# Kernel optimization log

Measured on AMD Instinct MI355X. Metric: run time of the kernel, lower is better.

## Reference

```python
import jax, jax.numpy as jnp
import numpy as np

N = 100000
E = 1600000
IN_F = 64
HID = 128
GC_OUT = 128
FEATS_OUT = 128


def _init_params(key):
    ks = jax.random.split(key, 6)
    s = 0.02
    return dict(
        W1=jax.random.normal(ks[0], (IN_F, HID), jnp.float32) * s,
        b1=jnp.zeros((HID,), jnp.float32),
        W2=jax.random.normal(ks[1], (HID, HID), jnp.float32) * s,
        b2=jnp.zeros((HID,), jnp.float32),
        Wgc=jax.random.normal(ks[2], (HID + IN_F, GC_OUT), jnp.float32) * s,
        bgc=jnp.zeros((GC_OUT,), jnp.float32),
        Wc=jax.random.normal(ks[3], (HID + GC_OUT, FEATS_OUT), jnp.float32) * s,
        bc=jnp.zeros((FEATS_OUT,), jnp.float32),
    )


def setup_inputs() -> dict:
    key = jax.random.key(0)
    k_f, k_e, k_p = jax.random.split(key, 3)
    inp = dict(
        feats=jax.random.normal(k_f, (N, IN_F), jnp.float32),
        edges=jax.random.randint(k_e, (2, E), 0, N, jnp.int64 if jax.config.read('jax_enable_x64') else jnp.int32),
        batch=jnp.zeros((N,), jnp.int32),
    )
    inp.update(_init_params(k_p))
    return inp


def _gcn_conv(x, edges, Wgc, bgc):
    # PyG GCNConv: linear transform, add self-loops, symmetric deg norm, scatter-add.
    n = x.shape[0]
    x = x @ Wgc  # [N, GC_OUT]
    loop = jnp.arange(n, dtype=edges.dtype)
    src = jnp.concatenate([edges[0], loop])
    dst = jnp.concatenate([edges[1], loop])
    deg = jax.ops.segment_sum(jnp.ones_like(dst, dtype=x.dtype), dst, num_segments=n)
    dinv = jnp.where(deg > 0, jax.lax.rsqrt(deg), 0.0)
    norm = dinv[src] * dinv[dst]  # [E+N]
    msg = x[src] * norm[:, None]  # gather + scale (memory-bound)
    agg = jax.ops.segment_sum(msg, dst, num_segments=n)  # scatter-add
    return agg + bgc


def reference(feats, edges, batch, W1, b1, W2, b2, Wgc, bgc, Wc, bc):
    elu = jax.nn.elu
    nfeats = elu(elu(feats @ W1 + b1) @ W2 + b2)  # fcnn
    gc_in = jnp.concatenate([nfeats, feats], axis=1)  # inject_input_to_gc
    gc_feats = _gcn_conv(gc_in, edges, Wgc, bgc)
    out_feats = elu(jnp.concatenate([nfeats, gc_feats], axis=1) @ Wc + bc)
    return (out_feats, edges, batch)
```

## Files before the change

### kernel.cpp

```cpp
#include <hip/hip_runtime.h>
#include <hip/hip_bf16.h>
#include <hip/hip_fp8.h>

constexpr int NN = 100000;
constexpr int NE = 1600000;

constexpr int SH1  = 9;
constexpr int NB1  = (NN + 511) >> SH1;
constexpr int EB   = 8192;
constexpr int NBLK = (NE + EB - 1) / EB;
constexpr int NH   = NB1 * NBLK;

constexpr float FP8_SCL  = 128.f;
constexpr float FP8_ISCL = 1.f / 128.f;

typedef __bf16 bf16_t;
typedef bf16_t bf16x8 __attribute__((ext_vector_type(8)));
typedef bf16_t bf16x4 __attribute__((ext_vector_type(4)));
typedef float  f32x4  __attribute__((ext_vector_type(4)));
typedef float  f32x2  __attribute__((ext_vector_type(2)));

__device__ inline float elu_fast(float v) {
  return v > 0.f ? v : (__expf(v) - 1.f);
}

__device__ inline unsigned char f_to_fp8(float v) {
  __hip_fp8_e4m3 q(v);
  return q.__x;
}
template<int SEL>
__device__ inline float fp8_to_f(unsigned int word) {
#if __has_builtin(__builtin_amdgcn_cvt_f32_fp8)
  return __builtin_amdgcn_cvt_f32_fp8(word, SEL);
#else
  __hip_fp8_e4m3 t; t.__x = (word >> (8 * SEL)) & 0xff; return (float)t;
#endif
}
template<bool W>
__device__ inline f32x2 fp8pk2(unsigned int word) {
#if __has_builtin(__builtin_amdgcn_cvt_pk_f32_fp8)
  return __builtin_amdgcn_cvt_pk_f32_fp8((int)word, W);
#else
  f32x2 o; o.x = fp8_to_f<W ? 2 : 0>(word); o.y = fp8_to_f<W ? 3 : 1>(word); return o;
#endif
}
__device__ inline void fp8x8_add(float* acc, uint2 v) {
  f32x2 p0 = fp8pk2<false>(v.x);
  f32x2 p1 = fp8pk2<true >(v.x);
  f32x2 p2 = fp8pk2<false>(v.y);
  f32x2 p3 = fp8pk2<true >(v.y);
  acc[0] += p0.x; acc[1] += p0.y;
  acc[2] += p1.x; acc[3] += p1.y;
  acc[4] += p2.x; acc[5] += p2.y;
  acc[6] += p3.x; acc[7] += p3.y;
}
__device__ inline void fp8x8_fma(float* acc, uint2 v, float s) {
  f32x2 p0 = fp8pk2<false>(v.x);
  f32x2 p1 = fp8pk2<true >(v.x);
  f32x2 p2 = fp8pk2<false>(v.y);
  f32x2 p3 = fp8pk2<true >(v.y);
  acc[0] += p0.x * s; acc[1] += p0.y * s;
  acc[2] += p1.x * s; acc[3] += p1.y * s;
  acc[4] += p2.x * s; acc[5] += p2.y * s;
  acc[6] += p3.x * s; acc[7] += p3.y * s;
}

constexpr int SB = 256;

__global__ void scan_blk(const int* __restrict__ in, int* __restrict__ incl,
                         int* __restrict__ bsum, int n) {
  __shared__ int sm[SB];
  int i = blockIdx.x * SB + threadIdx.x;
  int v = (i < n) ? in[i] : 0;
  sm[threadIdx.x] = v;
  __syncthreads();
  for (int off = 1; off < SB; off <<= 1) {
    int t = (threadIdx.x >= off) ? sm[threadIdx.x - off] : 0;
    __syncthreads();
    sm[threadIdx.x] += t;
    __syncthreads();
  }
  if (i < n) incl[i] = sm[threadIdx.x];
  if (threadIdx.x == SB - 1) bsum[blockIdx.x] = sm[SB - 1];
}

__global__ void scan_top(int* __restrict__ bsum, int nb) {
  __shared__ int sm[512];
  int t = threadIdx.x;
  int v = (t < nb) ? bsum[t] : 0;
  sm[t] = v;
  __syncthreads();
  for (int off = 1; off < 512; off <<= 1) {
    int u = (t >= off) ? sm[t - off] : 0;
    __syncthreads();
    sm[t] += u;
    __syncthreads();
  }
  if (t < nb) bsum[t] = sm[t] - v;
}

__global__ void scan_add(const int* __restrict__ incl, const int* __restrict__ in,
                         const int* __restrict__ bsum, int* __restrict__ outoff, int n) {
  int i = blockIdx.x * SB + threadIdx.x;
  if (i < n) {
    int off = bsum[blockIdx.x];
    outoff[i] = off + incl[i] - in[i];
    if (i == n - 1) outoff[n] = off + incl[i];
  }
}


__global__ __launch_bounds__(256) void histA(const int* __restrict__ dst,
                                             int* __restrict__ H, int e) {
  __shared__ int h[NB1];
  for (int i = threadIdx.x; i < NB1; i += 256) h[i] = 0;
  __syncthreads();
  int base = blockIdx.x * EB;
  int end = min(base + EB, e);
  for (int i = base + threadIdx.x; i < end; i += 256)
    atomicAdd(&h[dst[i] >> SH1], 1);
  __syncthreads();
  for (int i = threadIdx.x; i < NB1; i += 256)
    H[i * NBLK + blockIdx.x] = h[i];
}

__global__ void boff_k(const int* __restrict__ Hoff, int* __restrict__ boff) {
  int i = blockIdx.x * blockDim.x + threadIdx.x;
  if (i < NB1) boff[i] = Hoff[i * NBLK];
  if (i == NB1) boff[NB1] = NE;
}

__global__ __launch_bounds__(256) void scatterA(
    const int* __restrict__ src, const int* __restrict__ dst,
    const int* __restrict__ Hoff, unsigned long long* __restrict__ ebuf, int e) {
  __shared__ int cur[NB1];
  for (int i = threadIdx.x; i < NB1; i += 256)
    cur[i] = Hoff[i * NBLK + blockIdx.x];
  __syncthreads();
  int base = blockIdx.x * EB;
  int end = min(base + EB, e);
  for (int i = base + threadIdx.x; i < end; i += 256) {
    int d = dst[i], s = src[i];
    int pos = atomicAdd(&cur[d >> SH1], 1);
    ebuf[pos] = ((unsigned long long)(unsigned)d << 32) | (unsigned)s;
  }
}


__global__ __launch_bounds__(512) void bfin(const unsigned long long* __restrict__ ebuf,
                                            const int* __restrict__ boff,
                                            int* __restrict__ row_off, float* __restrict__ dinv,
                                            int* __restrict__ csr, int n) {
  __shared__ int cnt[512];
  __shared__ int loc[512];
  const int tid = threadIdx.x;
  const int b = blockIdx.x;
  cnt[tid] = 0;
  __syncthreads();
  const int e0 = boff[b], e1 = boff[b + 1];
  for (int e = e0 + tid; e < e1; e += 512)
    atomicAdd(&cnt[(int)(ebuf[e] >> 32) & 511], 1);
  __syncthreads();
  loc[tid] = cnt[tid];
  __syncthreads();
  for (int off = 1; off < 512; off <<= 1) {
    int t = (tid >= off) ? loc[tid - off] : 0;
    __syncthreads();
    loc[tid] += t;
    __syncthreads();
  }
  const int excl = loc[tid] - cnt[tid];
  const int node = (b << SH1) + tid;
  if (node < n) {
    row_off[node] = boff[b] + excl;
    dinv[node] = rsqrtf((float)cnt[tid] + 1.0f);
  }
  if (b == NB1 - 1 && tid == 0) row_off[n] = NE;
  cnt[tid] = boff[b] + excl;
  __syncthreads();
  for (int e = e0 + tid; e < e1; e += 512) {
    unsigned long long v = ebuf[e];
    int dl = (int)(v >> 32) & 511;
    int s  = (int)(v & 0xffffffffu);
    int slot = atomicAdd(&cnt[dl], 1);
    csr[slot] = s;
  }
}


__global__ void i2f4_k(const int4* __restrict__ in, float4* __restrict__ out, int n4) {
  int i = blockIdx.x * blockDim.x + threadIdx.x;
  if (i < n4) {
    int4 v = in[i];
    out[i] = make_float4((float)v.x, (float)v.y, (float)v.z, (float)v.w);
  }
}

__global__ void wprep4(const float* __restrict__ W1, const float* __restrict__ W2,
                       const float* __restrict__ Wgc, const float* __restrict__ Wc,
                       bf16_t* __restrict__ Wf) {
  int idx = blockIdx.x * blockDim.x + threadIdx.x;
  const float* W; int base;
  if      (idx < 8192)  { W = W1;  base = 0; }
  else if (idx < 24576) { W = W2;  base = 8192; }
  else if (idx < 49152) { W = Wgc; base = 24576; }
  else                  { W = Wc;  base = 49152; }
  int il   = idx - base;
  int j    = il & 7;
  int lane = (il >> 3) & 63;
  int c    = (il >> 9) & 7;
  int kt   = il >> 12;
  int k    = kt * 32 + (lane >> 4) * 8 + j;
  int col  = c * 16 + (lane & 15);
  Wf[idx] = (bf16_t)W[(size_t)k * 128 + col];
}

__global__ __launch_bounds__(256) void mf_dense123(
    const float* __restrict__ A, const bf16_t* __restrict__ W1f, const float* __restrict__ b1,
    const bf16_t* __restrict__ W2f, const float* __restrict__ b2,
    const bf16_t* __restrict__ Wgf, const float* __restrict__ dinv_g,
    bf16_t* __restrict__ h2out, unsigned char* __restrict__ xqout, int n)
{
  __shared__ __align__(16) char h1s[64 * 256];
  const int tid  = threadIdx.x;
  const int wv   = tid >> 6;
  const int lane = tid & 63;
  const int r    = lane & 15;
  const int kb   = lane >> 4;
  const int row0 = blockIdx.x * 64 + wv * 16;

  const bf16x8* W1V = (const bf16x8*)W1f;
  const bf16x8* W2V = (const bf16x8*)W2f;
  const bf16x8* WgV = (const bf16x8*)Wgf;

  f32x4 acc[8];
  #pragma unroll
  for (int c = 0; c < 8; ++c) acc[c] = (f32x4){0.f, 0.f, 0.f, 0.f};

  #pragma unroll
  for (int kt = 0; kt < 2; ++kt) {
    const int kofs = kt * 32 + kb * 8;
    int row = row0 + r; if (row >= n) row = n - 1;
    const float* fp = A + (size_t)row * 64 + kofs;
    float4 u = *(const float4*)fp;
    float4 v = *(const float4*)(fp + 4);
    bf16x8 a = (bf16x8){(bf16_t)u.x, (bf16_t)u.y, (bf16_t)u.z, (bf16_t)u.w,
                        (bf16_t)v.x, (bf16_t)v.y, (bf16_t)v.z, (bf16_t)v.w};
    #pragma unroll
    for (int c = 0; c < 8; ++c) {
      bf16x8 b = W1V[(kt * 8 + c) * 64 + lane];
      acc[c] = __builtin_amdgcn_mfma_f32_16x16x32_bf16(a, b, acc[c], 0, 0, 0);
    }
  }

  #pragma unroll
  for (int c = 0; c < 8; ++c) {
    const int col = c * 16 + r;
    const float bv = b1[col];
    #pragma unroll
    for (int q = 0; q < 4; ++q) {
      int rloc = wv * 16 + kb * 4 + q;
      float v = elu_fast(acc[c][q] + bv);
      int off = (rloc * 256 + col * 2) ^ ((rloc & 7) << 4);
      *(bf16_t*)(h1s + off) = (bf16_t)v;
    }
  }

  #pragma unroll
  for (int c = 0; c < 8; ++c) acc[c] = (f32x4){0.f, 0.f, 0.f, 0.f};

  #pragma unroll
  for (int kt = 0; kt < 4; ++kt) {
    const int kbyte = (kt * 32 + kb * 8) * 2;
    int rloc = wv * 16 + r;
    int off = (rloc * 256 + kbyte) ^ ((rloc & 7) << 4);
    bf16x8 a = *(const bf16x8*)(h1s + off);
    #pragma unroll
    for (int c = 0; c < 8; ++c) {
      bf16x8 b = W2V[(kt * 8 + c) * 64 + lane];
      acc[c] = __builtin_amdgcn_mfma_f32_16x16x32_bf16(a, b, acc[c], 0, 0, 0);
    }
  }

  #pragma unroll
  for (int c = 0; c < 8; ++c) {
    const int col = c * 16 + r;
    const float bv = b2[col];
    #pragma unroll
    for (int q = 0; q < 4; ++q) {
      int row  = row0 + kb * 4 + q;
      int rloc = wv * 16 + kb * 4 + q;
      float v = elu_fast(acc[c][q] + bv);
      int off = (rloc * 256 + col * 2) ^ ((rloc & 7) << 4);
      *(bf16_t*)(h1s + off) = (bf16_t)v;
      if (row < n) h2out[(size_t)row * 128 + col] = (bf16_t)v;
    }
  }

  #pragma unroll
  for (int c = 0; c < 8; ++c) acc[c] = (f32x4){0.f, 0.f, 0.f, 0.f};

  #pragma unroll
  for (int kt = 0; kt < 6; ++kt) {
    const int kofs = kt * 32 + kb * 8;
    bf16x8 a;
    if (kofs < 128) {
      int rloc = wv * 16 + r;
      int off = (rloc * 256 + kofs * 2) ^ ((rloc & 7) << 4);
      a = *(const bf16x8*)(h1s + off);
    } else {
      int row = row0 + r; if (row >= n) row = n - 1;
      const float* fp = A + (size_t)row * 64 + (kofs - 128);
      float4 u = *(const float4*)fp;
      float4 v = *(const float4*)(fp + 4);
      a = (bf16x8){(bf16_t)u.x, (bf16_t)u.y, (bf16_t)u.z, (bf16_t)u.w,
                   (bf16_t)v.x, (bf16_t)v.y, (bf16_t)v.z, (bf16_t)v.w};
    }
    #pragma unroll
    for (int c = 0; c < 8; ++c) {
      bf16x8 b = WgV[(kt * 8 + c) * 64 + lane];
      acc[c] = __builtin_amdgcn_mfma_f32_16x16x32_bf16(a, b, acc[c], 0, 0, 0);
    }
  }

  float dv[4];
  #pragma unroll
  for (int q = 0; q < 4; ++q) {
    int row = row0 + kb * 4 + q;
    dv[q] = (row < n) ? dinv_g[row] * FP8_SCL : 0.f;
  }
  #pragma unroll
  for (int c = 0; c < 8; ++c) {
    const int col = c * 16 + r;
    #pragma unroll
    for (int q = 0; q < 4; ++q) {
      int row = row0 + kb * 4 + q;
      if (row < n)
        xqout[(size_t)row * 128 + col] = f_to_fp8(acc[c][q] * dv[q]);
    }
  }
}

template<int K1, int K2, bool DOELU, int OMODE>
__global__ __launch_bounds__(256) void mf_dense(
    const bf16_t* __restrict__ A1, const bf16_t* __restrict__ A2b,
    const bf16_t* __restrict__ Wf, const float* __restrict__ bias,
    bf16_t* __restrict__ outb, float* __restrict__ outf, int n)
{
  constexpr int K   = K1 + K2;
  constexpr int NKT = K / 32;

  const int tid  = threadIdx.x;
  const int wv   = tid >> 6;
  const int lane = tid & 63;
  const int r    = lane & 15;
  const int kb   = lane >> 4;
  const int row0 = blockIdx.x * 64 + wv * 16;

  f32x4 acc[8];
  #pragma unroll
  for (int c = 0; c < 8; ++c) acc[c] = (f32x4){0.f, 0.f, 0.f, 0.f};

  const bf16x8* WfV = (const bf16x8*)Wf;

  #pragma unroll
  for (int kt = 0; kt < NKT; ++kt) {
    const int kofs = kt * 32 + kb * 8;
    int row = row0 + r; if (row >= n) row = n - 1;
    bf16x8 a;
    if (kofs < K1) a = *(const bf16x8*)(A1 + (size_t)row * K1 + kofs);
    else           a = *(const bf16x8*)(A2b + (size_t)row * K2 + (kofs - K1));
    #pragma unroll
    for (int c = 0; c < 8; ++c) {
      bf16x8 b = WfV[(kt * 8 + c) * 64 + lane];
      acc[c] = __builtin_amdgcn_mfma_f32_16x16x32_bf16(a, b, acc[c], 0, 0, 0);
    }
  }

  #pragma unroll
  for (int c = 0; c < 8; ++c) {
    const int col = c * 16 + r;
    const float bv = bias ? bias[col] : 0.f;
    #pragma unroll
    for (int q = 0; q < 4; ++q) {
      int row = row0 + kb * 4 + q;
      if (row < n) {
        float v = acc[c][q] + bv;
        if (DOELU) v = elu_fast(v);
        if (OMODE == 0) outb[(size_t)row * 128 + col] = (bf16_t)v;
        else            outf[(size_t)row * 128 + col] = v;
      }
    }
  }
}

__global__ __launch_bounds__(256) void gcn_agg6(
    const int* __restrict__ row_off, const int* __restrict__ csr,
    const float* __restrict__ dinv, const unsigned char* __restrict__ xq,
    const float* __restrict__ bgc, bf16_t* __restrict__ agg, int n)
{
  int w = (int)((blockIdx.x * (unsigned)blockDim.x + threadIdx.x) >> 6);
  if (w >= n) return;
  const int lane = threadIdx.x & 63;
  const int g  = lane >> 4;
  const int li = lane & 15;

  float acc[8];
  #pragma unroll
  for (int j = 0; j < 8; ++j) acc[j] = 0.f;

  if (g == 0) {
    uint2 sv = ((const uint2*)(xq + (size_t)w * 128))[li];
    fp8x8_add(acc, sv);
  }

  const int e0 = row_off[w], e1 = row_off[w + 1];
  int e = e0;
  for (; e + 16 <= e1; e += 16) {
    #pragma unroll
    for (int u = 0; u < 4; ++u) {
      int s = csr[e + 4 * u + g];
      uint2 v = ((const uint2*)(xq + (size_t)s * 128))[li];
      fp8x8_add(acc, v);
    }
  }
  for (; e < e1; e += 4) {
    int idx = e + g;
    int cidx = idx < e1 ? idx : e1 - 1;
    int s = csr[cidx];
    float coef = idx < e1 ? 1.f : 0.f;
    uint2 v = ((const uint2*)(xq + (size_t)s * 128))[li];
    fp8x8_fma(acc, v, coef);
  }

  #pragma unroll
  for (int j = 0; j < 8; ++j) {
    acc[j] += __shfl_xor(acc[j], 16);
    acc[j] += __shfl_xor(acc[j], 32);
  }

  if (g == 0) {
    const float sc = dinv[w] * FP8_ISCL;
    f32x4 b0 = ((const f32x4*)bgc)[2 * li];
    f32x4 b1 = ((const f32x4*)bgc)[2 * li + 1];
    bf16x8 o;
    o[0] = (bf16_t)(acc[0] * sc + b0[0]); o[1] = (bf16_t)(acc[1] * sc + b0[1]);
    o[2] = (bf16_t)(acc[2] * sc + b0[2]); o[3] = (bf16_t)(acc[3] * sc + b0[3]);
    o[4] = (bf16_t)(acc[4] * sc + b1[0]); o[5] = (bf16_t)(acc[5] * sc + b1[1]);
    o[6] = (bf16_t)(acc[6] * sc + b1[2]); o[7] = (bf16_t)(acc[7] * sc + b1[3]);
    ((bf16x8*)(agg + (size_t)w * 128))[li] = o;
  }
}


extern "C" void kernel_launch(void* const* d_in, const int* in_sizes, int n_in,
                              void* d_out, int out_size, void* d_ws, size_t ws_size,
                              hipStream_t stream) {
  (void)in_sizes; (void)n_in; (void)out_size; (void)ws_size;
  const float* feats = (const float*)d_in[0];
  const int*   edges = (const int*)d_in[1];
  const int*   batch = (const int*)d_in[2];
  const float* W1  = (const float*)d_in[3];
  const float* b1  = (const float*)d_in[4];
  const float* W2  = (const float*)d_in[5];
  const float* b2  = (const float*)d_in[6];
  const float* Wgc = (const float*)d_in[7];
  const float* bgc = (const float*)d_in[8];
  const float* Wc  = (const float*)d_in[9];
  const float* bc  = (const float*)d_in[10];
  float* out = (float*)d_out;

  bf16_t* h2b  = (bf16_t*)d_ws;
  bf16_t* aggb = h2b  + (size_t)NN * 128;
  unsigned char* xq8 = (unsigned char*)(aggb + (size_t)NN * 128);
  float*  dinv = (float*)(xq8 + (size_t)NN * 128);
  bf16_t* wall = (bf16_t*)(dinv + NN);
  bf16_t* w1f  = wall;
  bf16_t* w2f  = wall + 8192;
  bf16_t* wgcf = wall + 24576;
  bf16_t* wcf  = wall + 49152;

  int* scr     = (int*)d_out;
  int* csr_src = scr;
  int* row_off = csr_src + NE;
  int* H       = row_off + NN + 1;
  int* Hincl   = H + NH;
  int* Hoff    = Hincl + NH;
  int* boff    = Hoff + NH + 1;
  int* bsum2   = boff + NB1 + 1;
  unsigned long long* ebuf =
      (unsigned long long*)(((uintptr_t)(bsum2 + 512) + 7) & ~(uintptr_t)7);

  const int* esrc = edges;
  const int* edst = edges + NE;

  const int nscH = (NH + SB - 1) / SB;

  histA   <<<NBLK, 256, 0, stream>>>(edst, H, NE);
  scan_blk<<<nscH, SB, 0, stream>>>(H, Hincl, bsum2, NH);
  scan_top<<<1, 512, 0, stream>>>(bsum2, nscH);
  scan_add<<<nscH, SB, 0, stream>>>(Hincl, H, bsum2, Hoff, NH);
  boff_k  <<<1, 256, 0, stream>>>(Hoff, boff);
  scatterA<<<NBLK, 256, 0, stream>>>(esrc, edst, Hoff, ebuf, NE);
  bfin    <<<NB1, 512, 0, stream>>>(ebuf, boff, row_off, dinv, csr_src, NN);

  wprep4<<<320, 256, 0, stream>>>(W1, W2, Wgc, Wc, wall);

  const int nb = (NN + 63) / 64;
  mf_dense123<<<nb, 256, 0, stream>>>(feats, w1f, b1, w2f, b2, wgcf, dinv, h2b, xq8, NN);

  long long wthreads = (long long)NN * 64;
  gcn_agg6<<<(int)((wthreads + 255) / 256), 256, 0, stream>>>(
      row_off, csr_src, dinv, xq8, bgc, aggb, NN);

  mf_dense<128, 128, true, 1><<<nb, 256, 0, stream>>>(
      h2b, aggb, wcf, bc, nullptr, out, NN);

  size_t off = (size_t)NN * 128;
  i2f4_k<<<(2 * NE / 4 + 255) / 256, 256, 0, stream>>>(
      (const int4*)edges, (float4*)(out + off), 2 * NE / 4);
  i2f4_k<<<(NN / 4 + 255) / 256, 256, 0, stream>>>(
      (const int4*)batch, (float4*)(out + off + (size_t)2 * NE), NN / 4);
}
```

Baseline: 203.0 us.

## Stage pre-swizzled weights through LDS in chunks for dense MFMA kernels

Both dense kernels now copy the pre-swizzled bf16 weight fragments into a 16KB shared buffer one chunk at a time (two k-tiles per chunk) with block-wide barriers. The MFMA B operands are then read from LDS instead of being loaded by every wave from global memory or L2. The fused dense123 kernel is restructured into one loop over six chunks, with the bias+ELU epilogues placed at the layer boundaries. This adds two barriers per chunk and extra LDS use, which may lower occupancy and serialises load and compute within each chunk.

```diff
diff --git a/kernel.cpp b/kernel.cpp
--- a/kernel.cpp
+++ b/kernel.cpp
@@ -216,12 +216,13 @@
 }
 
 __global__ __launch_bounds__(256) void mf_dense123(
-    const float* __restrict__ A, const bf16_t* __restrict__ W1f, const float* __restrict__ b1,
-    const bf16_t* __restrict__ W2f, const float* __restrict__ b2,
-    const bf16_t* __restrict__ Wgf, const float* __restrict__ dinv_g,
+    const float* __restrict__ A, const bf16_t* __restrict__ Wall,
+    const float* __restrict__ b1, const float* __restrict__ b2,
+    const float* __restrict__ dinv_g,
     bf16_t* __restrict__ h2out, unsigned char* __restrict__ xqout, int n)
 {
   __shared__ __align__(16) char h1s[64 * 256];
+  __shared__ __align__(16) char wbuf[16384];
   const int tid  = threadIdx.x;
   const int wv   = tid >> 6;
   const int lane = tid & 63;
@@ -229,97 +230,88 @@
   const int kb   = lane >> 4;
   const int row0 = blockIdx.x * 64 + wv * 16;
 
-  const bf16x8* W1V = (const bf16x8*)W1f;
-  const bf16x8* W2V = (const bf16x8*)W2f;
-  const bf16x8* WgV = (const bf16x8*)Wgf;
-
   f32x4 acc[8];
   #pragma unroll
   for (int c = 0; c < 8; ++c) acc[c] = (f32x4){0.f, 0.f, 0.f, 0.f};
 
-  #pragma unroll
-  for (int kt = 0; kt < 2; ++kt) {
-    const int kofs = kt * 32 + kb * 8;
-    int row = row0 + r; if (row >= n) row = n - 1;
-    const float* fp = A + (size_t)row * 64 + kofs;
-    float4 u = *(const float4*)fp;
-    float4 v = *(const float4*)(fp + 4);
-    bf16x8 a = (bf16x8){(bf16_t)u.x, (bf16_t)u.y, (bf16_t)u.z, (bf16_t)u.w,
-                        (bf16_t)v.x, (bf16_t)v.y, (bf16_t)v.z, (bf16_t)v.w};
+  int rowA = row0 + r; if (rowA >= n) rowA = n - 1;
+  const int rloc = wv * 16 + r;
+
+  for (int ch = 0; ch < 6; ++ch) {
+    __syncthreads();
+    {
+      const char* src = (const char*)Wall + ch * 16384;
+      #pragma unroll
+      for (int k = 0; k < 4; ++k) {
+        float4 v = *(const float4*)(src + k * 4096 + tid * 16);
+        *(float4*)(wbuf + k * 4096 + tid * 16) = v;
+      }
+    }
+    __syncthreads();
+
     #pragma unroll
-    for (int c = 0; c < 8; ++c) {
-      bf16x8 b = W1V[(kt * 8 + c) * 64 + lane];
-      acc[c] = __builtin_amdgcn_mfma_f32_16x16x32_bf16(a, b, acc[c], 0, 0, 0);
-    }
-  }
-
-  #pragma unroll
-  for (int c = 0; c < 8; ++c) {
-    const int col = c * 16 + r;
-    const float bv = b1[col];
-    #pragma unroll
-    for (int q = 0; q < 4; ++q) {
-      int rloc = wv * 16 + kb * 4 + q;
-      float v = elu_fast(acc[c][q] + bv);
-      int off = (rloc * 256 + col * 2) ^ ((rloc & 7) << 4);
-      *(bf16_t*)(h1s + off) = (bf16_t)v;
-    }
-  }
-
-  #pragma unroll
-  for (int c = 0; c < 8; ++c) acc[c] = (f32x4){0.f, 0.f, 0.f, 0.f};
-
-  #pragma unroll
-  for (int kt = 0; kt < 4; ++kt) {
-    const int kbyte = (kt * 32 + kb * 8) * 2;
-    int rloc = wv * 16 + r;
-    int off = (rloc * 256 + kbyte) ^ ((rloc & 7) << 4);
-    bf16x8 a = *(const bf16x8*)(h1s + off);
-    #pragma unroll
-    for (int c = 0; c < 8; ++c) {
-      bf16x8 b = W2V[(kt * 8 + c) * 64 + lane];
-      acc[c] = __builtin_amdgcn_mfma_f32_16x16x32_bf16(a, b, acc[c], 0, 0, 0);
-    }
-  }
-
-  #pragma unroll
-  for (int c = 0; c < 8; ++c) {
-    const int col = c * 16 + r;
-    const float bv = b2[col];
-    #pragma unroll
-    for (int q = 0; q < 4; ++q) {
-      int row  = row0 + kb * 4 + q;
-      int rloc = wv * 16 + kb * 4 + q;
-      float v = elu_fast(acc[c][q] + bv);
-      int off = (rloc * 256 + col * 2) ^ ((rloc & 7) << 4);
-      *(bf16_t*)(h1s + off) = (bf16_t)v;
-      if (row < n) h2out[(size_t)row * 128 + col] = (bf16_t)v;
-    }
-  }
-
-  #pragma unroll
-  for (int c = 0; c < 8; ++c) acc[c] = (f32x4){0.f, 0.f, 0.f, 0.f};
-
-  #pragma unroll
-  for (int kt = 0; kt < 6; ++kt) {
-    const int kofs = kt * 32 + kb * 8;
-    bf16x8 a;
-    if (kofs < 128) {
-      int rloc = wv * 16 + r;
-      int off = (rloc * 256 + kofs * 2) ^ ((rloc & 7) << 4);
-      a = *(const bf16x8*)(h1s + off);
-    } else {
-      int row = row0 + r; if (row >= n) row = n - 1;
-      const float* fp = A + (size_t)row * 64 + (kofs - 128);
-      float4 u = *(const float4*)fp;
-      float4 v = *(const float4*)(fp + 4);
-      a = (bf16x8){(bf16_t)u.x, (bf16_t)u.y, (bf16_t)u.z, (bf16_t)u.w,
-                   (bf16_t)v.x, (bf16_t)v.y, (bf16_t)v.z, (bf16_t)v.w};
-    }
-    #pragma unroll
-    for (int c = 0; c < 8; ++c) {
-      bf16x8 b = WgV[(kt * 8 + c) * 64 + lane];
-      acc[c] = __builtin_amdgcn_mfma_f32_16x16x32_bf16(a, b, acc[c], 0, 0, 0);
+    for (int lk = 0; lk < 2; ++lk) {
+      const int gkt = ch * 2 + lk;
+      bf16x8 a;
+      if (gkt < 2) {
+        const float* fp = A + (size_t)rowA * 64 + gkt * 32 + kb * 8;
+        float4 u = *(const float4*)fp;
+        float4 v = *(const float4*)(fp + 4);
+        a = (bf16x8){(bf16_t)u.x, (bf16_t)u.y, (bf16_t)u.z, (bf16_t)u.w,
+                     (bf16_t)v.x, (bf16_t)v.y, (bf16_t)v.z, (bf16_t)v.w};
+      } else if (gkt < 6) {
+        int kbyte = ((gkt - 2) * 32 + kb * 8) * 2;
+        int off = (rloc * 256 + kbyte) ^ ((rloc & 7) << 4);
+        a = *(const bf16x8*)(h1s + off);
+      } else {
+        int kofs = (gkt - 6) * 32 + kb * 8;
+        if (kofs < 128) {
+          int off = (rloc * 256 + kofs * 2) ^ ((rloc & 7) << 4);
+          a = *(const bf16x8*)(h1s + off);
+        } else {
+          const float* fp = A + (size_t)rowA * 64 + (kofs - 128);
+          float4 u = *(const float4*)fp;
+          float4 v = *(const float4*)(fp + 4);
+          a = (bf16x8){(bf16_t)u.x, (bf16_t)u.y, (bf16_t)u.z, (bf16_t)u.w,
+                       (bf16_t)v.x, (bf16_t)v.y, (bf16_t)v.z, (bf16_t)v.w};
+        }
+      }
+      #pragma unroll
+      for (int c = 0; c < 8; ++c) {
+        bf16x8 b = *(const bf16x8*)(wbuf + ((lk * 8 + c) * 64 + lane) * 16);
+        acc[c] = __builtin_amdgcn_mfma_f32_16x16x32_bf16(a, b, acc[c], 0, 0, 0);
+      }
+      if (gkt == 1) {
+        #pragma unroll
+        for (int c = 0; c < 8; ++c) {
+          const int col = c * 16 + r;
+          const float bv = b1[col];
+          #pragma unroll
+          for (int q = 0; q < 4; ++q) {
+            int rl = wv * 16 + kb * 4 + q;
+            float v = elu_fast(acc[c][q] + bv);
+            int off = (rl * 256 + col * 2) ^ ((rl & 7) << 4);
+            *(bf16_t*)(h1s + off) = (bf16_t)v;
+          }
+          acc[c] = (f32x4){0.f, 0.f, 0.f, 0.f};
+        }
+      } else if (gkt == 5) {
+        #pragma unroll
+        for (int c = 0; c < 8; ++c) {
+          const int col = c * 16 + r;
+          const float bv = b2[col];
+          #pragma unroll
+          for (int q = 0; q < 4; ++q) {
+            int row = row0 + kb * 4 + q;
+            int rl  = wv * 16 + kb * 4 + q;
+            float v = elu_fast(acc[c][q] + bv);
+            int off = (rl * 256 + col * 2) ^ ((rl & 7) << 4);
+            *(bf16_t*)(h1s + off) = (bf16_t)v;
+            if (row < n) h2out[(size_t)row * 128 + col] = (bf16_t)v;
+          }
+          acc[c] = (f32x4){0.f, 0.f, 0.f, 0.f};
+        }
+      }
     }
   }
 
@@ -341,15 +333,12 @@
   }
 }
 
-template<int K1, int K2, bool DOELU, int OMODE>
-__global__ __launch_bounds__(256) void mf_dense(
-    const bf16_t* __restrict__ A1, const bf16_t* __restrict__ A2b,
+__global__ __launch_bounds__(256) void mf_dense_s(
+    const bf16_t* __restrict__ A1, const bf16_t* __restrict__ A2,
     const bf16_t* __restrict__ Wf, const float* __restrict__ bias,
-    bf16_t* __restrict__ outb, float* __restrict__ outf, int n)
+    float* __restrict__ outf, int n)
 {
-  constexpr int K   = K1 + K2;
-  constexpr int NKT = K / 32;
-
+  __shared__ __align__(16) char wbuf[16384];
   const int tid  = threadIdx.x;
   const int wv   = tid >> 6;
   const int lane = tid & 63;
@@ -361,34 +350,44 @@
   #pragma unroll
   for (int c = 0; c < 8; ++c) acc[c] = (f32x4){0.f, 0.f, 0.f, 0.f};
 
-  const bf16x8* WfV = (const bf16x8*)Wf;
-
-  #pragma unroll
-  for (int kt = 0; kt < NKT; ++kt) {
-    const int kofs = kt * 32 + kb * 8;
-    int row = row0 + r; if (row >= n) row = n - 1;
-    bf16x8 a;
-    if (kofs < K1) a = *(const bf16x8*)(A1 + (size_t)row * K1 + kofs);
-    else           a = *(const bf16x8*)(A2b + (size_t)row * K2 + (kofs - K1));
+  int rowA = row0 + r; if (rowA >= n) rowA = n - 1;
+
+  for (int ch = 0; ch < 4; ++ch) {
+    __syncthreads();
+    {
+      const char* src = (const char*)Wf + ch * 16384;
+      #pragma unroll
+      for (int k = 0; k < 4; ++k) {
+        float4 v = *(const float4*)(src + k * 4096 + tid * 16);
+        *(float4*)(wbuf + k * 4096 + tid * 16) = v;
+      }
+    }
+    __syncthreads();
+
     #pragma unroll
-    for (int c = 0; c < 8; ++c) {
-      bf16x8 b = WfV[(kt * 8 + c) * 64 + lane];
-      acc[c] = __builtin_amdgcn_mfma_f32_16x16x32_bf16(a, b, acc[c], 0, 0, 0);
+    for (int lk = 0; lk < 2; ++lk) {
+      const int gkt = ch * 2 + lk;
+      bf16x8 a;
+      if (gkt < 4) a = *(const bf16x8*)(A1 + (size_t)rowA * 128 + gkt * 32 + kb * 8);
+      else         a = *(const bf16x8*)(A2 + (size_t)rowA * 128 + (gkt - 4) * 32 + kb * 8);
+      #pragma unroll
+      for (int c = 0; c < 8; ++c) {
+        bf16x8 b = *(const bf16x8*)(wbuf + ((lk * 8 + c) * 64 + lane) * 16);
+        acc[c] = __builtin_amdgcn_mfma_f32_16x16x32_bf16(a, b, acc[c], 0, 0, 0);
+      }
     }
   }
 
   #pragma unroll
   for (int c = 0; c < 8; ++c) {
     const int col = c * 16 + r;
-    const float bv = bias ? bias[col] : 0.f;
+    const float bv = bias[col];
     #pragma unroll
     for (int q = 0; q < 4; ++q) {
       int row = row0 + kb * 4 + q;
       if (row < n) {
-        float v = acc[c][q] + bv;
-        if (DOELU) v = elu_fast(v);
-        if (OMODE == 0) outb[(size_t)row * 128 + col] = (bf16_t)v;
-        else            outf[(size_t)row * 128 + col] = v;
+        float v = elu_fast(acc[c][q] + bv);
+        outf[(size_t)row * 128 + col] = v;
       }
     }
   }
@@ -475,9 +474,6 @@
   unsigned char* xq8 = (unsigned char*)(aggb + (size_t)NN * 128);
   float*  dinv = (float*)(xq8 + (size_t)NN * 128);
   bf16_t* wall = (bf16_t*)(dinv + NN);
-  bf16_t* w1f  = wall;
-  bf16_t* w2f  = wall + 8192;
-  bf16_t* wgcf = wall + 24576;
   bf16_t* wcf  = wall + 49152;
 
   int* scr     = (int*)d_out;
@@ -507,14 +503,13 @@
   wprep4<<<320, 256, 0, stream>>>(W1, W2, Wgc, Wc, wall);
 
   const int nb = (NN + 63) / 64;
-  mf_dense123<<<nb, 256, 0, stream>>>(feats, w1f, b1, w2f, b2, wgcf, dinv, h2b, xq8, NN);
+  mf_dense123<<<nb, 256, 0, stream>>>(feats, wall, b1, b2, dinv, h2b, xq8, NN);
 
   long long wthreads = (long long)NN * 64;
   gcn_agg6<<<(int)((wthreads + 255) / 256), 256, 0, stream>>>(
       row_off, csr_src, dinv, xq8, bgc, aggb, NN);
 
-  mf_dense<128, 128, true, 1><<<nb, 256, 0, stream>>>(
-      h2b, aggb, wcf, bc, nullptr, out, NN);
+  mf_dense_s<<<nb, 256, 0, stream>>>(h2b, aggb, wcf, bc, out, NN);
 
   size_t off = (size_t)NN * 128;
   i2f4_k<<<(2 * NE / 4 + 255) / 256, 256, 0, stream>>>(
```

After: 177.3 us. 12.6% less time.
